# Kernel optimization log

Hardware: AMD Instinct MI355X
Metric: run time of the kernel (lower is better)

Reference implementation:

```python
import jax, jax.numpy as jnp
import numpy as np

ALPHA = 1.0
N, P, D = 8192, 128, 256
NUM_CLASSES = 128


def setup_inputs() -> dict:
    key = jax.random.key(0)
    kx, ky, kp = jax.random.split(key, 3)
    x = jax.random.normal(kx, (N, D), dtype=jnp.float32)
    y = jax.random.randint(ky, (N,), 0, NUM_CLASSES)
    prototypes = jax.random.normal(kp, (P, D), dtype=jnp.float32)
    return {"x": x, "y": y, "prototypes": prototypes}


def reference(x, y, prototypes):
    # (same math as the broadcasted sum((x-p)**2), expressed as a GEMM)
    x_sq = jnp.sum(x * x, axis=1, keepdims=True)          # [N, 1]
    p_sq = jnp.sum(prototypes * prototypes, axis=1)       # [P]
    dist = x_sq - 2.0 * jnp.einsum('nd,pd->np', x, prototypes) + p_sq[None, :]  # [N, P]

    # Torch code sets correct_mask[arange(N), y] = True, i.e. the "correct"
    # prototype is the one whose INDEX equals the class label y.
    n_idx = jnp.arange(dist.shape[0])
    d1 = dist[n_idx, y]                                    # [N] distance to correct prototype
    incorrect = jnp.where(jax.nn.one_hot(y, dist.shape[1], dtype=jnp.bool_),
                          jnp.inf, dist)
    d2 = jnp.min(incorrect, axis=1)                        # [N] min over wrong prototypes

    mu = (d1 - d2) / (d1 + d2)
    return jnp.mean(jax.nn.sigmoid(-ALPHA * mu))
```

## Files before the change

kernel.cpp:

```cpp
#include <hip/hip_runtime.h>
#include <math.h>

#define N_ROWS  8192
#define DIM     256
#define NPROTO  128
#define ROWS_PB 16
#define NBLK    (N_ROWS / ROWS_PB)

typedef float f32x4 __attribute__((ext_vector_type(4)));
typedef short s16x8 __attribute__((ext_vector_type(8)));

__device__ __forceinline__ unsigned short f2bf(float f) {
  unsigned int u = __float_as_uint(f);
  u += 0x7fffu + ((u >> 16) & 1u);
  return (unsigned short)(u >> 16);
}

__device__ __forceinline__ void gl_lds16(const void* g, void* l) {
  __builtin_amdgcn_global_load_lds(
      (const __attribute__((address_space(1))) void*)g,
      (__attribute__((address_space(3))) void*)l, 16, 0, 0);
}

__global__ __launch_bounds__(256) void glvq_prep_kernel(
    const float* __restrict__ proto, unsigned short* __restrict__ pbf,
    float* __restrict__ psq, float* __restrict__ out) {
  const int tid = blockIdx.x * 256 + threadIdx.x;
  const int row = tid >> 5;
  const int co  = tid & 31;
  const float4* p4 = (const float4*)proto;
  float4 a = p4[tid * 2];
  float4 b = p4[tid * 2 + 1];
  union { s16x8 v; unsigned short u[8]; } pk;
  pk.u[0] = f2bf(a.x); pk.u[1] = f2bf(a.y); pk.u[2] = f2bf(a.z); pk.u[3] = f2bf(a.w);
  pk.u[4] = f2bf(b.x); pk.u[5] = f2bf(b.y); pk.u[6] = f2bf(b.z); pk.u[7] = f2bf(b.w);
  const int slot = row * 32 + (co ^ (row & 7));
  *(s16x8*)&pbf[slot * 8] = pk.v;
  float s = a.x * a.x + a.y * a.y + a.z * a.z + a.w * a.w +
            b.x * b.x + b.y * b.y + b.z * b.z + b.w * b.w;
#pragma unroll
  for (int m = 1; m <= 16; m <<= 1) s += __shfl_xor(s, m);
  if (co == 0) psq[row] = s;
  if (tid == 0) out[0] = 0.f;
}

__global__ __launch_bounds__(256, 2) void glvq_kernel(
    const float* __restrict__ x, const int* __restrict__ y,
    const unsigned short* __restrict__ pbf, const float* __restrict__ psq_g,
    float* __restrict__ out) {
  __shared__ unsigned short pT[NPROTO * 256];
  __shared__ unsigned short xT[ROWS_PB * 256];
  __shared__ float psq[NPROTO];
  __shared__ float xsq[ROWS_PB];
  __shared__ int   ylds[ROWS_PB];
  __shared__ float red1[4 * ROWS_PB];
  __shared__ float red2[4 * ROWS_PB];

  const int t = threadIdx.x;
  const int r0 = blockIdx.x * ROWS_PB;

#pragma unroll
  for (int j = 0; j < 16; ++j) {
    int c = j * 256 + t;
    gl_lds16((const char*)pbf + (size_t)c * 16, (char*)pT + (size_t)c * 16);
  }
  if (t < NPROTO) psq[t] = psq_g[t];
  if (t < ROWS_PB) ylds[t] = y[r0 + t];

  {
    const int r = t >> 4, i = t & 15;
    const float4* xr = (const float4*)x + (size_t)(r0 + r) * 64 + i * 4;
    float4 v0 = xr[0], v1 = xr[1], v2 = xr[2], v3 = xr[3];
    union { s16x8 v; unsigned short u[8]; } pk0, pk1;
    pk0.u[0] = f2bf(v0.x); pk0.u[1] = f2bf(v0.y); pk0.u[2] = f2bf(v0.z); pk0.u[3] = f2bf(v0.w);
    pk0.u[4] = f2bf(v1.x); pk0.u[5] = f2bf(v1.y); pk0.u[6] = f2bf(v1.z); pk0.u[7] = f2bf(v1.w);
    pk1.u[0] = f2bf(v2.x); pk1.u[1] = f2bf(v2.y); pk1.u[2] = f2bf(v2.z); pk1.u[3] = f2bf(v2.w);
    pk1.u[4] = f2bf(v3.x); pk1.u[5] = f2bf(v3.y); pk1.u[6] = f2bf(v3.z); pk1.u[7] = f2bf(v3.w);
    const int r7 = r & 7;
    *(s16x8*)&xT[(r * 32 + ((2 * i) ^ r7)) * 8] = pk0.v;
    *(s16x8*)&xT[(r * 32 + ((2 * i + 1) ^ r7)) * 8] = pk1.v;
    float s = v0.x * v0.x + v0.y * v0.y + v0.z * v0.z + v0.w * v0.w +
              v1.x * v1.x + v1.y * v1.y + v1.z * v1.z + v1.w * v1.w +
              v2.x * v2.x + v2.y * v2.y + v2.z * v2.z + v2.w * v2.w +
              v3.x * v3.x + v3.y * v3.y + v3.z * v3.z + v3.w * v3.w;
#pragma unroll
    for (int m = 1; m <= 8; m <<= 1) s += __shfl_xor(s, m);
    if (i == 0) xsq[r] = s;
  }
  __syncthreads();

  const int l = t & 63;
  const int w = t >> 6;
  const int mq = l >> 4;
  const int mc = l & 15;
  const int m7 = mc & 7;
  f32x4 acc0 = {0.f, 0.f, 0.f, 0.f};
  f32x4 acc1 = {0.f, 0.f, 0.f, 0.f};
  const unsigned short* xbase = &xT[mc * 256];
  const unsigned short* b0p = &pT[(w * 32 + mc) * 256];
  const unsigned short* b1p = b0p + 16 * 256;
#pragma unroll
  for (int ks = 0; ks < 8; ++ks) {
    const int off = ((mq + 4 * ks) ^ m7) * 8;
    s16x8 af  = *(const s16x8*)(xbase + off);
    s16x8 bf0 = *(const s16x8*)(b0p + off);
    s16x8 bf1 = *(const s16x8*)(b1p + off);
    acc0 = __builtin_amdgcn_mfma_f32_16x16x32_bf16(af, bf0, acc0, 0, 0, 0);
    acc1 = __builtin_amdgcn_mfma_f32_16x16x32_bf16(af, bf1, acc1, 0, 0, 0);
  }

  const int p0i = w * 32 + mc;
  const int p1i = p0i + 16;
  const float pq0 = psq[p0i];
  const float pq1 = psq[p1i];
  float r1[4], r2[4];
#pragma unroll
  for (int reg = 0; reg < 4; ++reg) {
    int m = mq * 4 + reg;
    float xs = xsq[m];
    int ym = ylds[m];
    float d0 = xs + pq0 - 2.f * acc0[reg];
    float d1_ = xs + pq1 - 2.f * acc1[reg];
    float dd1 = 1e30f, dd2 = 1e30f;
    if (p0i == ym) dd1 = d0; else dd2 = d0;
    if (p1i == ym) dd1 = fminf(dd1, d1_); else dd2 = fminf(dd2, d1_);
    r1[reg] = dd1;
    r2[reg] = dd2;
  }
#pragma unroll
  for (int m = 1; m <= 8; m <<= 1) {
#pragma unroll
    for (int reg = 0; reg < 4; ++reg) {
      r1[reg] = fminf(r1[reg], __shfl_xor(r1[reg], m));
      r2[reg] = fminf(r2[reg], __shfl_xor(r2[reg], m));
    }
  }
  if (mc == 0) {
#pragma unroll
    for (int reg = 0; reg < 4; ++reg) {
      red1[w * ROWS_PB + mq * 4 + reg] = r1[reg];
      red2[w * ROWS_PB + mq * 4 + reg] = r2[reg];
    }
  }
  __syncthreads();

  if (t < ROWS_PB) {
    float d1 = 1e30f, d2 = 1e30f;
#pragma unroll
    for (int wv = 0; wv < 4; ++wv) {
      d1 = fminf(d1, red1[wv * ROWS_PB + t]);
      d2 = fminf(d2, red2[wv * ROWS_PB + t]);
    }
    float mu = (d1 - d2) / (d1 + d2);
    float s = 1.f / (1.f + __expf(mu));
#pragma unroll
    for (int m = 1; m <= 8; m <<= 1) s += __shfl_xor(s, m);
    if (t == 0) atomicAdd(out, s * (1.f / (float)N_ROWS));
  }
}

extern "C" void kernel_launch(void* const* d_in, const int* in_sizes, int n_in,
                              void* d_out, int out_size, void* d_ws, size_t ws_size,
                              hipStream_t stream) {
  const float* x = (const float*)d_in[0];
  const int* y = (const int*)d_in[1];
  const float* proto = (const float*)d_in[2];
  float* out = (float*)d_out;

  unsigned short* pbf = (unsigned short*)d_ws;
  float* psq = (float*)((char*)d_ws + NPROTO * DIM * 2);

  glvq_prep_kernel<<<16, 256, 0, stream>>>(proto, pbf, psq, out);
  glvq_kernel<<<NBLK, 256, 0, stream>>>(x, y, pbf, psq, out);
}
```

Before: 71.06 us.

## Move x bf16 conversion to prep kernel and give each wave all prototypes

The x-to-bf16 conversion and row-norm computation move into the prep kernel, which writes bf16 x and the squared norms to workspace. The main kernel now runs 256 blocks of 128 threads, each wave handling 16 rows against all 128 prototypes held in registers and accumulators. This lets each wave finish its distance reduction with shuffles alone and cuts block-level LDS reductions and syncs. Each block loads the full 64KB prototype tile into LDS for only 32 rows, and x now makes an extra global round trip through the workspace.

```diff
diff --git a/kernel.cpp b/kernel.cpp
--- a/kernel.cpp
+++ b/kernel.cpp
@@ -4,8 +4,6 @@
 #define N_ROWS  8192
 #define DIM     256
 #define NPROTO  128
-#define ROWS_PB 16
-#define NBLK    (N_ROWS / ROWS_PB)
 
 typedef float f32x4 __attribute__((ext_vector_type(4)));
 typedef short s16x8 __attribute__((ext_vector_type(8)));
@@ -22,63 +20,26 @@
       (__attribute__((address_space(3))) void*)l, 16, 0, 0);
 }
 
-__global__ __launch_bounds__(256) void glvq_prep_kernel(
-    const float* __restrict__ proto, unsigned short* __restrict__ pbf,
-    float* __restrict__ psq, float* __restrict__ out) {
-  const int tid = blockIdx.x * 256 + threadIdx.x;
-  const int row = tid >> 5;
-  const int co  = tid & 31;
-  const float4* p4 = (const float4*)proto;
-  float4 a = p4[tid * 2];
-  float4 b = p4[tid * 2 + 1];
-  union { s16x8 v; unsigned short u[8]; } pk;
-  pk.u[0] = f2bf(a.x); pk.u[1] = f2bf(a.y); pk.u[2] = f2bf(a.z); pk.u[3] = f2bf(a.w);
-  pk.u[4] = f2bf(b.x); pk.u[5] = f2bf(b.y); pk.u[6] = f2bf(b.z); pk.u[7] = f2bf(b.w);
-  const int slot = row * 32 + (co ^ (row & 7));
-  *(s16x8*)&pbf[slot * 8] = pk.v;
-  float s = a.x * a.x + a.y * a.y + a.z * a.z + a.w * a.w +
-            b.x * b.x + b.y * b.y + b.z * b.z + b.w * b.w;
-#pragma unroll
-  for (int m = 1; m <= 16; m <<= 1) s += __shfl_xor(s, m);
-  if (co == 0) psq[row] = s;
-  if (tid == 0) out[0] = 0.f;
-}
-
-__global__ __launch_bounds__(256, 2) void glvq_kernel(
-    const float* __restrict__ x, const int* __restrict__ y,
-    const unsigned short* __restrict__ pbf, const float* __restrict__ psq_g,
+__global__ __launch_bounds__(256) void glvq_prep(
+    const float* __restrict__ x, const float* __restrict__ proto,
+    unsigned short* __restrict__ xbf, float* __restrict__ xsq,
+    unsigned short* __restrict__ pbf, float* __restrict__ psq,
     float* __restrict__ out) {
-  __shared__ unsigned short pT[NPROTO * 256];
-  __shared__ unsigned short xT[ROWS_PB * 256];
-  __shared__ float psq[NPROTO];
-  __shared__ float xsq[ROWS_PB];
-  __shared__ int   ylds[ROWS_PB];
-  __shared__ float red1[4 * ROWS_PB];
-  __shared__ float red2[4 * ROWS_PB];
-
   const int t = threadIdx.x;
-  const int r0 = blockIdx.x * ROWS_PB;
-
-#pragma unroll
-  for (int j = 0; j < 16; ++j) {
-    int c = j * 256 + t;
-    gl_lds16((const char*)pbf + (size_t)c * 16, (char*)pT + (size_t)c * 16);
-  }
-  if (t < NPROTO) psq[t] = psq_g[t];
-  if (t < ROWS_PB) ylds[t] = y[r0 + t];
+  const int b = blockIdx.x;
 
   {
-    const int r = t >> 4, i = t & 15;
-    const float4* xr = (const float4*)x + (size_t)(r0 + r) * 64 + i * 4;
+    const int r = b * 16 + (t >> 4);
+    const int i = t & 15;
+    const float4* xr = (const float4*)x + (size_t)r * 64 + i * 4;
     float4 v0 = xr[0], v1 = xr[1], v2 = xr[2], v3 = xr[3];
     union { s16x8 v; unsigned short u[8]; } pk0, pk1;
     pk0.u[0] = f2bf(v0.x); pk0.u[1] = f2bf(v0.y); pk0.u[2] = f2bf(v0.z); pk0.u[3] = f2bf(v0.w);
     pk0.u[4] = f2bf(v1.x); pk0.u[5] = f2bf(v1.y); pk0.u[6] = f2bf(v1.z); pk0.u[7] = f2bf(v1.w);
     pk1.u[0] = f2bf(v2.x); pk1.u[1] = f2bf(v2.y); pk1.u[2] = f2bf(v2.z); pk1.u[3] = f2bf(v2.w);
     pk1.u[4] = f2bf(v3.x); pk1.u[5] = f2bf(v3.y); pk1.u[6] = f2bf(v3.z); pk1.u[7] = f2bf(v3.w);
-    const int r7 = r & 7;
-    *(s16x8*)&xT[(r * 32 + ((2 * i) ^ r7)) * 8] = pk0.v;
-    *(s16x8*)&xT[(r * 32 + ((2 * i + 1) ^ r7)) * 8] = pk1.v;
+    *(s16x8*)&xbf[(size_t)r * 256 + i * 16] = pk0.v;
+    *(s16x8*)&xbf[(size_t)r * 256 + i * 16 + 8] = pk1.v;
     float s = v0.x * v0.x + v0.y * v0.y + v0.z * v0.z + v0.w * v0.w +
               v1.x * v1.x + v1.y * v1.y + v1.z * v1.z + v1.w * v1.w +
               v2.x * v2.x + v2.y * v2.y + v2.z * v2.z + v2.w * v2.w +
@@ -87,76 +48,97 @@
     for (int m = 1; m <= 8; m <<= 1) s += __shfl_xor(s, m);
     if (i == 0) xsq[r] = s;
   }
+
+  if (b < 16) {
+    const int tid = b * 256 + t;
+    const int row = tid >> 5;
+    const int co  = tid & 31;
+    const float4* p4 = (const float4*)proto;
+    float4 a = p4[tid * 2];
+    float4 bb = p4[tid * 2 + 1];
+    union { s16x8 v; unsigned short u[8]; } pk;
+    pk.u[0] = f2bf(a.x);  pk.u[1] = f2bf(a.y);  pk.u[2] = f2bf(a.z);  pk.u[3] = f2bf(a.w);
+    pk.u[4] = f2bf(bb.x); pk.u[5] = f2bf(bb.y); pk.u[6] = f2bf(bb.z); pk.u[7] = f2bf(bb.w);
+    const int slot = row * 32 + (co ^ (row & 7));
+    *(s16x8*)&pbf[slot * 8] = pk.v;
+    float s = a.x * a.x + a.y * a.y + a.z * a.z + a.w * a.w +
+              bb.x * bb.x + bb.y * bb.y + bb.z * bb.z + bb.w * bb.w;
+#pragma unroll
+    for (int m = 1; m <= 16; m <<= 1) s += __shfl_xor(s, m);
+    if (co == 0) psq[row] = s;
+  }
+  if (b == 0 && t == 0) out[0] = 0.f;
+}
+
+__global__ __launch_bounds__(128) void glvq_main(
+    const unsigned short* __restrict__ xbf, const float* __restrict__ xsq_g,
+    const int* __restrict__ y, const unsigned short* __restrict__ pbf,
+    const float* __restrict__ psq_g, float* __restrict__ out) {
+  __shared__ unsigned short pT[NPROTO * 256];
+
+  const int t = threadIdx.x;
+#pragma unroll
+  for (int j = 0; j < 32; ++j) {
+    const int c = j * 128 + t;
+    gl_lds16((const char*)pbf + (size_t)c * 16, (char*)pT + (size_t)c * 16);
+  }
+
+  const int wv = t >> 6, l = t & 63, mq = l >> 4, mc = l & 15;
+  const int row_base = blockIdx.x * 32 + wv * 16;
+
+  float xs[4]; int yr[4];
+#pragma unroll
+  for (int reg = 0; reg < 4; ++reg) {
+    xs[reg] = xsq_g[row_base + mq * 4 + reg];
+    yr[reg] = y[row_base + mq * 4 + reg];
+  }
+  float pq[8];
+#pragma unroll
+  for (int j = 0; j < 8; ++j) pq[j] = psq_g[j * 16 + mc];
+
+  s16x8 afr[8];
+  const unsigned short* xrow = xbf + (size_t)(row_base + mc) * 256;
+#pragma unroll
+  for (int ks = 0; ks < 8; ++ks)
+    afr[ks] = *(const s16x8*)(xrow + ks * 32 + mq * 8);
+
   __syncthreads();
 
-  const int l = t & 63;
-  const int w = t >> 6;
-  const int mq = l >> 4;
-  const int mc = l & 15;
+  f32x4 acc[8];
+#pragma unroll
+  for (int j = 0; j < 8; ++j) acc[j] = (f32x4){0.f, 0.f, 0.f, 0.f};
   const int m7 = mc & 7;
-  f32x4 acc0 = {0.f, 0.f, 0.f, 0.f};
-  f32x4 acc1 = {0.f, 0.f, 0.f, 0.f};
-  const unsigned short* xbase = &xT[mc * 256];
-  const unsigned short* b0p = &pT[(w * 32 + mc) * 256];
-  const unsigned short* b1p = b0p + 16 * 256;
 #pragma unroll
   for (int ks = 0; ks < 8; ++ks) {
-    const int off = ((mq + 4 * ks) ^ m7) * 8;
-    s16x8 af  = *(const s16x8*)(xbase + off);
-    s16x8 bf0 = *(const s16x8*)(b0p + off);
-    s16x8 bf1 = *(const s16x8*)(b1p + off);
-    acc0 = __builtin_amdgcn_mfma_f32_16x16x32_bf16(af, bf0, acc0, 0, 0, 0);
-    acc1 = __builtin_amdgcn_mfma_f32_16x16x32_bf16(af, bf1, acc1, 0, 0, 0);
+#pragma unroll
+    for (int j = 0; j < 8; ++j) {
+      const int p = j * 16 + mc;
+      const s16x8 bf = *(const s16x8*)&pT[(p * 32 + ((4 * ks + mq) ^ m7)) * 8];
+      acc[j] = __builtin_amdgcn_mfma_f32_16x16x32_bf16(afr[ks], bf, acc[j], 0, 0, 0);
+    }
   }
 
-  const int p0i = w * 32 + mc;
-  const int p1i = p0i + 16;
-  const float pq0 = psq[p0i];
-  const float pq1 = psq[p1i];
-  float r1[4], r2[4];
+  float ssum = 0.f;
 #pragma unroll
   for (int reg = 0; reg < 4; ++reg) {
-    int m = mq * 4 + reg;
-    float xs = xsq[m];
-    int ym = ylds[m];
-    float d0 = xs + pq0 - 2.f * acc0[reg];
-    float d1_ = xs + pq1 - 2.f * acc1[reg];
-    float dd1 = 1e30f, dd2 = 1e30f;
-    if (p0i == ym) dd1 = d0; else dd2 = d0;
-    if (p1i == ym) dd1 = fminf(dd1, d1_); else dd2 = fminf(dd2, d1_);
-    r1[reg] = dd1;
-    r2[reg] = dd2;
-  }
-#pragma unroll
-  for (int m = 1; m <= 8; m <<= 1) {
-#pragma unroll
-    for (int reg = 0; reg < 4; ++reg) {
-      r1[reg] = fminf(r1[reg], __shfl_xor(r1[reg], m));
-      r2[reg] = fminf(r2[reg], __shfl_xor(r2[reg], m));
-    }
-  }
-  if (mc == 0) {
-#pragma unroll
-    for (int reg = 0; reg < 4; ++reg) {
-      red1[w * ROWS_PB + mq * 4 + reg] = r1[reg];
-      red2[w * ROWS_PB + mq * 4 + reg] = r2[reg];
-    }
-  }
-  __syncthreads();
-
-  if (t < ROWS_PB) {
     float d1 = 1e30f, d2 = 1e30f;
 #pragma unroll
-    for (int wv = 0; wv < 4; ++wv) {
-      d1 = fminf(d1, red1[wv * ROWS_PB + t]);
-      d2 = fminf(d2, red2[wv * ROWS_PB + t]);
+    for (int j = 0; j < 8; ++j) {
+      const float d = xs[reg] + pq[j] - 2.f * acc[j][reg];
+      if (j * 16 + mc == yr[reg]) d1 = d; else d2 = fminf(d2, d);
     }
-    float mu = (d1 - d2) / (d1 + d2);
-    float s = 1.f / (1.f + __expf(mu));
 #pragma unroll
-    for (int m = 1; m <= 8; m <<= 1) s += __shfl_xor(s, m);
-    if (t == 0) atomicAdd(out, s * (1.f / (float)N_ROWS));
+    for (int m = 1; m <= 8; m <<= 1) {
+      d1 = fminf(d1, __shfl_xor(d1, m));
+      d2 = fminf(d2, __shfl_xor(d2, m));
+    }
+    const float mu = (d1 - d2) / (d1 + d2);
+    ssum += 1.f / (1.f + __expf(mu));
   }
+  if (mc != 0) ssum = 0.f;
+  ssum += __shfl_xor(ssum, 16);
+  ssum += __shfl_xor(ssum, 32);
+  if (l == 0) atomicAdd(out, ssum * (1.f / (float)N_ROWS));
 }
 
 extern "C" void kernel_launch(void* const* d_in, const int* in_sizes, int n_in,
@@ -167,9 +149,12 @@
   const float* proto = (const float*)d_in[2];
   float* out = (float*)d_out;
 
-  unsigned short* pbf = (unsigned short*)d_ws;
-  float* psq = (float*)((char*)d_ws + NPROTO * DIM * 2);
+  char* ws = (char*)d_ws;
+  unsigned short* pbf = (unsigned short*)ws;
+  unsigned short* xbf = (unsigned short*)(ws + 65536);
+  float* xsq = (float*)(ws + 65536 + (size_t)N_ROWS * DIM * 2);
+  float* psq = (float*)(ws + 65536 + (size_t)N_ROWS * DIM * 2 + N_ROWS * 4);
 
-  glvq_prep_kernel<<<16, 256, 0, stream>>>(proto, pbf, psq, out);
-  glvq_kernel<<<NBLK, 256, 0, stream>>>(x, y, pbf, psq, out);
+  glvq_prep<<<512, 256, 0, stream>>>(x, proto, xbf, xsq, pbf, psq, out);
+  glvq_main<<<256, 128, 0, stream>>>(xbf, xsq, y, pbf, psq, out);
 }
```

After: 71.90 us. No clear change (+1.2%).
